# Kernel optimization log

Measured on AMD Instinct MI355X. Metric: run time of the kernel, lower is better.

Reference implementation:

```python
import jax, jax.numpy as jnp
import numpy as np

N, L, C, H = 8, 2048, 512, 512
C_HALF = max(C // 2, 1)


def setup_inputs() -> dict:
    key = jax.random.key(0)
    ks = jax.random.split(key, 11)
    s = 0.02
    return {
        "x": jax.random.normal(ks[0], (N, L, C), dtype=jnp.float32),
        "theta_w": jax.random.normal(ks[1], (C, H), dtype=jnp.float32) * s,
        "theta_b": jax.random.normal(ks[2], (H,), dtype=jnp.float32) * s,
        "phi_w": jax.random.normal(ks[3], (C, H), dtype=jnp.float32) * s,
        "phi_b": jax.random.normal(ks[4], (H,), dtype=jnp.float32) * s,
        "psi_w": jax.random.normal(ks[5], (C, H), dtype=jnp.float32) * s,
        "psi_b": jax.random.normal(ks[6], (H,), dtype=jnp.float32) * s,
        "r1_w": jax.random.normal(ks[7], (H, C_HALF), dtype=jnp.float32) * s,
        "r1_b": jax.random.normal(ks[8], (C_HALF,), dtype=jnp.float32) * s,
        "r2_w": jax.random.normal(ks[9], (C_HALF, C), dtype=jnp.float32) * s,
        "r2_b": jax.random.normal(ks[10], (C,), dtype=jnp.float32) * s,
    }


def reference(x, theta_w, theta_b, phi_w, phi_b, psi_w, psi_b, r1_w, r1_b, r2_w, r2_b):
    # projections: [n, L, h]
    x_t = x @ theta_w + theta_b
    x_ph = x @ phi_w + phi_b
    x_psi = x @ psi_w + psi_b
    # unscaled attention: phi @ theta^T -> [n, L, L], softmax over last dim
    attn = jax.nn.softmax(jnp.einsum("nlh,nmh->nlm", x_ph, x_t), axis=2)
    x_add = jnp.einsum("nlm,nmh->nlh", attn, x_psi)
    # recover MLP with LeakyReLU(0.2) then Tanh, residual add
    h1 = jax.nn.leaky_relu(x_add @ r1_w + r1_b, negative_slope=0.2)
    h2 = jnp.tanh(h1 @ r2_w + r2_b)
    return x + h2
```

## Files before the change

### kernel.cpp

```cpp
#include <hip/hip_runtime.h>
#include <hip/hip_bf16.h>

typedef __bf16 bf16x8 __attribute__((ext_vector_type(8)));
typedef float  f32x4  __attribute__((ext_vector_type(4)));
typedef __attribute__((address_space(3))) unsigned int       lds_uint;
typedef __attribute__((address_space(1))) const unsigned int glb_uint;

__device__ __forceinline__ unsigned short f2bf(float f) {
    unsigned int u = __float_as_uint(f);
    u += 0x7fffu + ((u >> 16) & 1u);
    return (unsigned short)(u >> 16);
}
__device__ __forceinline__ float tanh_fast(float x) {
    float e = __expf(-2.0f * fabsf(x));
    float r = (1.0f - e) / (1.0f + e);
    return copysignf(r, x);
}
__device__ __forceinline__ unsigned char f2fp8(float v) {
    return (unsigned char)(__builtin_amdgcn_cvt_pk_fp8_f32(v, 0.0f, 0, false) & 0xff);
}

__global__ __launch_bounds__(256) void prep(
    const float* __restrict__ x,
    const float* __restrict__ theta_w, const float* __restrict__ phi_w,
    const float* __restrict__ psi_w,   const float* __restrict__ r1_w,
    const float* __restrict__ r2_w,
    const float* __restrict__ theta_b, const float* __restrict__ phi_b,
    const float* __restrict__ psi_b,
    unsigned char* __restrict__ xb8, unsigned char* __restrict__ wCat8T,
    unsigned short* __restrict__ r1T, unsigned short* __restrict__ r2T,
    float* __restrict__ bCat) {
    const int b = blockIdx.x, t = threadIdx.x;
    if (b < 8192) {
        long i = ((long)b * 256 + t) * 4;
        float4 f = *(const float4*)(x + i);
        int w = __builtin_amdgcn_cvt_pk_fp8_f32(f.x, f.y, 0, false);
        w = __builtin_amdgcn_cvt_pk_fp8_f32(f.z, f.w, w, true);
        *(unsigned int*)(xb8 + i) = (unsigned int)w;
    } else if (b < 11264) {
        const int sel = (b - 8192) >> 10;
        const int idx = ((b - 8192) & 1023) * 256 + t;
        const float* w = sel == 0 ? theta_w : (sel == 1 ? phi_w : psi_w);
        const int r = idx >> 9, c = idx & 511;
        wCat8T[(long)(sel * 512 + c) * 512 + r] = f2fp8(w[idx] * 16.0f);
    } else if (b < 11776) {
        const int idx = (b - 11264) * 256 + t;
        const int r = idx >> 8, c = idx & 255;
        r1T[(long)c * 512 + r] = f2bf(r1_w[idx]);
    } else if (b < 12288) {
        const int idx = (b - 11776) * 256 + t;
        const int r = idx >> 9, c = idx & 511;
        r2T[(long)c * 256 + r] = f2bf(r2_w[idx]);
    } else {
        const int i = (b - 12288) * 256 + t;
        if (i < 1536)
            bCat[i] = i < 512 ? theta_b[i] : (i < 1024 ? phi_b[i - 512] : psi_b[i - 1024]);
    }
}

__global__ __launch_bounds__(256) void softmax_fp8(unsigned short* __restrict__ S) {
    const size_t row = (size_t)blockIdx.y * 2048 + blockIdx.x;
    unsigned short* p = S + row * 2048;
    const int t = threadIdx.x;
    uint4 raw = *(uint4*)(p + t * 8);
    unsigned int w[4] = {raw.x, raw.y, raw.z, raw.w};
    float v[8];
#pragma unroll
    for (int i = 0; i < 4; ++i) {
        v[2 * i]     = __uint_as_float((w[i] & 0xffffu) << 16);
        v[2 * i + 1] = __uint_as_float(w[i] & 0xffff0000u);
    }
    float mx = v[0];
#pragma unroll
    for (int i = 1; i < 8; ++i) mx = fmaxf(mx, v[i]);
#pragma unroll
    for (int off = 32; off > 0; off >>= 1) mx = fmaxf(mx, __shfl_xor(mx, off));
    __shared__ float red[8];
    const int wave = t >> 6, lane = t & 63;
    if (lane == 0) red[wave] = mx;
    __syncthreads();
    mx = fmaxf(fmaxf(red[0], red[1]), fmaxf(red[2], red[3]));
    float s = 0.0f;
#pragma unroll
    for (int i = 0; i < 8; ++i) { v[i] = __expf(v[i] - mx); s += v[i]; }
#pragma unroll
    for (int off = 32; off > 0; off >>= 1) s += __shfl_xor(s, off);
    if (lane == 0) red[4 + wave] = s;
    __syncthreads();
    s = red[4] + red[5] + red[6] + red[7];
    const float inv = 1.0f / s;
    int o0 = __builtin_amdgcn_cvt_pk_fp8_f32(v[0] * inv, v[1] * inv, 0, false);
    o0 = __builtin_amdgcn_cvt_pk_fp8_f32(v[2] * inv, v[3] * inv, o0, true);
    int o1 = __builtin_amdgcn_cvt_pk_fp8_f32(v[4] * inv, v[5] * inv, 0, false);
    o1 = __builtin_amdgcn_cvt_pk_fp8_f32(v[6] * inv, v[7] * inv, o1, true);
    uint2 ov; ov.x = (unsigned int)o0; ov.y = (unsigned int)o1;
    *(uint2*)((unsigned char*)p + t * 8) = ov;
}

template <int MODE>
__global__ __launch_bounds__(256) void gemm_fp8(
    const unsigned char* __restrict__ A,
    const unsigned char* __restrict__ Bt,
    const float* __restrict__ bias,
    unsigned short* __restrict__ outB,
    unsigned char* __restrict__ outT,
    unsigned char* __restrict__ outP,
    unsigned char* __restrict__ outV,
    int K, int ldaB, int ldbB, int ldc, long sA, long sB, long sC) {
    __shared__ unsigned char As[128 * 128];
    __shared__ unsigned char Bs[128 * 128];

    const int tid  = threadIdx.x;
    const int lane = tid & 63, wave = tid >> 6;
    const int m16  = lane & 15, quad = lane >> 4;
    const int wm   = (wave >> 1) << 6, wn = (wave & 1) << 6;
    const int m0   = blockIdx.x << 7, n0 = blockIdx.y << 7;

    const int srow = lane >> 3;
    const int uswz = (lane & 7) ^ srow;

    const unsigned char* Abase = A  + (long)blockIdx.z * sA + (long)m0 * ldaB;
    const unsigned char* Bbase = Bt + (long)blockIdx.z * sB + (long)n0 * ldbB;
    const int stR = (wave << 5) + srow;
    const long gA0 = (long)stR * ldaB + (uswz << 4);
    const long gB0 = (long)stR * ldbB + (uswz << 4);

    f32x4 acc[4][4] = {};

    for (int k0 = 0; k0 < K; k0 += 128) {
        __syncthreads();
#pragma unroll
        for (int i = 0; i < 4; ++i) {
            const unsigned char* gp = Abase + gA0 + (long)(i << 3) * ldaB + k0;
            unsigned char* lp = &As[(((wave << 5) + (i << 3)) << 7)];
            __builtin_amdgcn_global_load_lds((glb_uint*)gp, (lds_uint*)lp, 16, 0, 0);
        }
#pragma unroll
        for (int i = 0; i < 4; ++i) {
            const unsigned char* gp = Bbase + gB0 + (long)(i << 3) * ldbB + k0;
            unsigned char* lp = &Bs[(((wave << 5) + (i << 3)) << 7)];
            __builtin_amdgcn_global_load_lds((glb_uint*)gp, (lds_uint*)lp, 16, 0, 0);
        }
        __syncthreads();
#pragma unroll
        for (int ks = 0; ks < 4; ++ks) {
            long af[4], bg[4];
#pragma unroll
            for (int f = 0; f < 4; ++f) {
                const int m = wm + (f << 4) + m16;
                const int n = wn + (f << 4) + m16;
                const int c = (ks << 2) + quad;
                af[f] = *(const long*)&As[(m << 7) + ((c ^ ((m & 7) << 1)) << 3)];
                bg[f] = *(const long*)&Bs[(n << 7) + ((c ^ ((n & 7) << 1)) << 3)];
            }
#pragma unroll
            for (int fi = 0; fi < 4; ++fi)
#pragma unroll
                for (int fj = 0; fj < 4; ++fj)
                    acc[fi][fj] = __builtin_amdgcn_mfma_f32_16x16x32_fp8_fp8(
                        af[fi], bg[fj], acc[fi][fj], 0, 0, 0);
        }
    }

    const long zC = (long)blockIdx.z * sC;
#pragma unroll
    for (int fj = 0; fj < 4; ++fj) {
        const int col = n0 + wn + (fj << 4) + m16;
        float bv = 0.0f;
        if (MODE == 0) bv = bias[col];
#pragma unroll
        for (int fi = 0; fi < 4; ++fi) {
#pragma unroll
            for (int r = 0; r < 4; ++r) {
                const int row = m0 + wm + (fi << 4) + (quad << 2) + r;
                if (MODE == 0) {
                    const float v = acc[fi][fj][r] * 0.0625f + bv;
                    const unsigned char b8 = f2fp8(v);
                    const int sel = col >> 9, cb = col & 511;
                    if (sel == 0)      outT[(long)row * 512 + cb] = b8;
                    else if (sel == 1) outP[(long)row * 512 + cb] = b8;
                    else {
                        const int z = row >> 11, l = row & 2047;
                        outV[((long)z * 512 + cb) * 2048 + l] = b8;
                    }
                } else {
                    outB[zC + (long)row * ldc + col] = f2bf(acc[fi][fj][r]);
                }
            }
        }
    }
}

template <int MODE>
__global__ __launch_bounds__(256) void gemm128(
    const unsigned short* __restrict__ A,
    const unsigned short* __restrict__ Bt,
    const float* __restrict__ bias,
    const float* __restrict__ resid,
    unsigned short* __restrict__ outB,
    float* __restrict__ outF,
    int K, int lda, int ldb, int ldc) {
    __shared__ __bf16 As[128 * 64];
    __shared__ __bf16 Bs[128 * 64];

    const int tid  = threadIdx.x;
    const int lane = tid & 63, wave = tid >> 6;
    const int m16  = lane & 15, quad = lane >> 4;
    const int wm   = (wave >> 1) << 6, wn = (wave & 1) << 6;
    const int m0   = blockIdx.x << 7, n0 = blockIdx.y << 7;

    const int srow  = lane >> 3;
    const int uswz  = (lane & 7) ^ srow;

    const unsigned short* Abase = A  + (long)m0 * lda;
    const unsigned short* Bbase = Bt + (long)n0 * ldb;
    const int stR = (wave << 5) + srow;
    const long gA0 = (long)stR * lda + (uswz << 3);
    const long gB0 = (long)stR * ldb + (uswz << 3);

    f32x4 acc[4][4] = {};

    for (int k0 = 0; k0 < K; k0 += 64) {
        __syncthreads();
#pragma unroll
        for (int i = 0; i < 4; ++i) {
            const unsigned short* gp = Abase + gA0 + (long)(i << 3) * lda + k0;
            __bf16* lp = &As[(((wave << 5) + (i << 3)) << 6)];
            __builtin_amdgcn_global_load_lds((glb_uint*)gp, (lds_uint*)lp, 16, 0, 0);
        }
#pragma unroll
        for (int i = 0; i < 4; ++i) {
            const unsigned short* gp = Bbase + gB0 + (long)(i << 3) * ldb + k0;
            __bf16* lp = &Bs[(((wave << 5) + (i << 3)) << 6)];
            __builtin_amdgcn_global_load_lds((glb_uint*)gp, (lds_uint*)lp, 16, 0, 0);
        }
        __syncthreads();
#pragma unroll
        for (int ks = 0; ks < 2; ++ks) {
            bf16x8 af[4], bg[4];
#pragma unroll
            for (int f = 0; f < 4; ++f) {
                const int m  = wm + (f << 4) + m16;
                const int n  = wn + (f << 4) + m16;
                const int cu = (ks << 2) + quad;
                af[f] = *(const bf16x8*)&As[(m << 6) + ((cu ^ (m & 7)) << 3)];
                bg[f] = *(const bf16x8*)&Bs[(n << 6) + ((cu ^ (n & 7)) << 3)];
            }
#pragma unroll
            for (int fi = 0; fi < 4; ++fi)
#pragma unroll
                for (int fj = 0; fj < 4; ++fj)
                    acc[fi][fj] = __builtin_amdgcn_mfma_f32_16x16x32_bf16(
                        af[fi], bg[fj], acc[fi][fj], 0, 0, 0);
        }
    }

#pragma unroll
    for (int fj = 0; fj < 4; ++fj) {
        const int col = n0 + wn + (fj << 4) + m16;
        const float bv = bias[col];
#pragma unroll
        for (int fi = 0; fi < 4; ++fi) {
#pragma unroll
            for (int r = 0; r < 4; ++r) {
                const int row = m0 + wm + (fi << 4) + (quad << 2) + r;
                float v = acc[fi][fj][r] + bv;
                const long idx = (long)row * ldc + col;
                if (MODE == 2) {
                    v = v > 0.0f ? v : 0.2f * v;
                    outB[idx] = f2bf(v);
                } else {
                    outF[idx] = tanh_fast(v) + resid[idx];
                }
            }
        }
    }
}

extern "C" void kernel_launch(void* const* d_in, const int* in_sizes, int n_in,
                              void* d_out, int out_size, void* d_ws, size_t ws_size,
                              hipStream_t stream) {
    const float* x       = (const float*)d_in[0];
    const float* theta_w = (const float*)d_in[1];
    const float* theta_b = (const float*)d_in[2];
    const float* phi_w   = (const float*)d_in[3];
    const float* phi_b   = (const float*)d_in[4];
    const float* psi_w   = (const float*)d_in[5];
    const float* psi_b   = (const float*)d_in[6];
    const float* r1_w    = (const float*)d_in[7];
    const float* r1_b    = (const float*)d_in[8];
    const float* r2_w    = (const float*)d_in[9];
    const float* r2_b    = (const float*)d_in[10];
    float* out = (float*)d_out;

    constexpr int  N = 8, L = 2048, C = 512, H = 512, CH = 256;
    constexpr long NL = (long)N * L;

    char* p = (char*)d_ws;
    auto alloc = [&](size_t bytes) { void* q = (void*)p; p += bytes; return q; };
    unsigned char*  xb8    = (unsigned char*)alloc(NL * C);
    unsigned char*  TH8    = (unsigned char*)alloc(NL * H);
    unsigned char*  PH8    = (unsigned char*)alloc(NL * H);
    unsigned char*  VT8    = (unsigned char*)alloc((long)N * H * L);
    unsigned short* xadd   = (unsigned short*)alloc(NL * H * 2);
    unsigned short* h1     = (unsigned short*)alloc(NL * CH * 2);
    unsigned char*  wCat8T = (unsigned char*)alloc((long)1536 * 512);
    unsigned short* r1T    = (unsigned short*)alloc((long)H * CH * 2);
    unsigned short* r2T    = (unsigned short*)alloc((long)CH * C * 2);
    float*          bCat   = (float*)alloc(1536 * 4 + 256);
    unsigned short* S      = (unsigned short*)alloc((long)N * L * L * 2);

    prep<<<12294, 256, 0, stream>>>(x, theta_w, phi_w, psi_w, r1_w, r2_w,
                                    theta_b, phi_b, psi_b, xb8, wCat8T, r1T, r2T, bCat);

    gemm_fp8<0><<<dim3(NL / 128, 1536 / 128, 1), 256, 0, stream>>>(
        xb8, wCat8T, bCat, nullptr, TH8, PH8, VT8,
        C, C, C, 0, 0, 0, 0);

    gemm_fp8<1><<<dim3(L / 128, L / 128, N), 256, 0, stream>>>(
        PH8, TH8, nullptr, S, nullptr, nullptr, nullptr,
        H, H, H, L, (long)L * H, (long)L * H, (long)L * L);

    softmax_fp8<<<dim3(L, N), 256, 0, stream>>>(S);

    gemm_fp8<1><<<dim3(L / 128, H / 128, N), 256, 0, stream>>>(
        (const unsigned char*)S, VT8, nullptr, xadd, nullptr, nullptr, nullptr,
        L, 2 * L, L, H, (long)L * 2 * L, (long)H * L, (long)L * H);

    gemm128<2><<<dim3(NL / 128, CH / 128, 1), 256, 0, stream>>>(
        xadd, r1T, r1_b, nullptr, h1, nullptr, H, H, H, CH);

    gemm128<3><<<dim3(NL / 128, C / 128, 1), 256, 0, stream>>>(
        h1, r2T, r2_b, x, nullptr, out, CH, CH, CH, C);
}
```

Baseline: 262.5 us.

## Move recover MLP GEMMs to fp8, store scores as fp16, vectorize V-transpose stores

Quantizes the recover-MLP weights and intermediate activations (x_add, h1) to fp8, so the two MLP GEMMs run through the fp8 MFMA kernel instead of the bf16 one. The scores buffer changes from bf16 to fp16, and the projection epilogue for the V part now packs four fp8 values per 32-bit store instead of scattering single bytes. The aim is to halve the memory traffic and raise MFMA throughput in the tail GEMMs and to cut store transactions in the projection. In exchange it adds fp8 quantization error to the MLP path, and fp16 scores may overflow for large logits.

```diff
diff --git a/kernel.cpp b/kernel.cpp
--- a/kernel.cpp
+++ b/kernel.cpp
@@ -1,16 +1,10 @@
 #include <hip/hip_runtime.h>
 #include <hip/hip_bf16.h>
 
-typedef __bf16 bf16x8 __attribute__((ext_vector_type(8)));
-typedef float  f32x4  __attribute__((ext_vector_type(4)));
+typedef float f32x4 __attribute__((ext_vector_type(4)));
 typedef __attribute__((address_space(3))) unsigned int       lds_uint;
 typedef __attribute__((address_space(1))) const unsigned int glb_uint;
 
-__device__ __forceinline__ unsigned short f2bf(float f) {
-    unsigned int u = __float_as_uint(f);
-    u += 0x7fffu + ((u >> 16) & 1u);
-    return (unsigned short)(u >> 16);
-}
 __device__ __forceinline__ float tanh_fast(float x) {
     float e = __expf(-2.0f * fabsf(x));
     float r = (1.0f - e) / (1.0f + e);
@@ -18,6 +12,17 @@
 }
 __device__ __forceinline__ unsigned char f2fp8(float v) {
     return (unsigned char)(__builtin_amdgcn_cvt_pk_fp8_f32(v, 0.0f, 0, false) & 0xff);
+}
+__device__ __forceinline__ unsigned short f2h(float v) {
+    _Float16 h = (_Float16)v;
+    unsigned short u;
+    __builtin_memcpy(&u, &h, 2);
+    return u;
+}
+__device__ __forceinline__ float h2f(unsigned short u) {
+    _Float16 h;
+    __builtin_memcpy(&h, &u, 2);
+    return (float)h;
 }
 
 __global__ __launch_bounds__(256) void prep(
@@ -28,7 +33,7 @@
     const float* __restrict__ theta_b, const float* __restrict__ phi_b,
     const float* __restrict__ psi_b,
     unsigned char* __restrict__ xb8, unsigned char* __restrict__ wCat8T,
-    unsigned short* __restrict__ r1T, unsigned short* __restrict__ r2T,
+    unsigned char* __restrict__ r1T8, unsigned char* __restrict__ r2T8,
     float* __restrict__ bCat) {
     const int b = blockIdx.x, t = threadIdx.x;
     if (b < 8192) {
@@ -46,11 +51,11 @@
     } else if (b < 11776) {
         const int idx = (b - 11264) * 256 + t;
         const int r = idx >> 8, c = idx & 255;
-        r1T[(long)c * 512 + r] = f2bf(r1_w[idx]);
+        r1T8[(long)c * 512 + r] = f2fp8(r1_w[idx] * 16.0f);
     } else if (b < 12288) {
         const int idx = (b - 11776) * 256 + t;
         const int r = idx >> 9, c = idx & 511;
-        r2T[(long)c * 256 + r] = f2bf(r2_w[idx]);
+        r2T8[(long)c * 256 + r] = f2fp8(r2_w[idx] * 16.0f);
     } else {
         const int i = (b - 12288) * 256 + t;
         if (i < 1536)
@@ -67,8 +72,8 @@
     float v[8];
 #pragma unroll
     for (int i = 0; i < 4; ++i) {
-        v[2 * i]     = __uint_as_float((w[i] & 0xffffu) << 16);
-        v[2 * i + 1] = __uint_as_float(w[i] & 0xffff0000u);
+        v[2 * i]     = h2f((unsigned short)(w[i] & 0xffffu));
+        v[2 * i + 1] = h2f((unsigned short)(w[i] >> 16));
     }
     float mx = v[0];
 #pragma unroll
@@ -102,10 +107,12 @@
     const unsigned char* __restrict__ A,
     const unsigned char* __restrict__ Bt,
     const float* __restrict__ bias,
-    unsigned short* __restrict__ outB,
-    unsigned char* __restrict__ outT,
-    unsigned char* __restrict__ outP,
+    const float* __restrict__ resid,
+    unsigned short* __restrict__ outH,
+    unsigned char* __restrict__ out8,
+    unsigned char* __restrict__ out8b,
     unsigned char* __restrict__ outV,
+    float* __restrict__ outF,
     int K, int ldaB, int ldbB, int ldc, long sA, long sB, long sC) {
     __shared__ unsigned char As[128 * 128];
     __shared__ unsigned char Bs[128 * 128];
@@ -163,116 +170,68 @@
     }
 
     const long zC = (long)blockIdx.z * sC;
-#pragma unroll
-    for (int fj = 0; fj < 4; ++fj) {
-        const int col = n0 + wn + (fj << 4) + m16;
-        float bv = 0.0f;
-        if (MODE == 0) bv = bias[col];
-#pragma unroll
-        for (int fi = 0; fi < 4; ++fi) {
-#pragma unroll
-            for (int r = 0; r < 4; ++r) {
-                const int row = m0 + wm + (fi << 4) + (quad << 2) + r;
-                if (MODE == 0) {
-                    const float v = acc[fi][fj][r] * 0.0625f + bv;
-                    const unsigned char b8 = f2fp8(v);
-                    const int sel = col >> 9, cb = col & 511;
-                    if (sel == 0)      outT[(long)row * 512 + cb] = b8;
-                    else if (sel == 1) outP[(long)row * 512 + cb] = b8;
-                    else {
-                        const int z = row >> 11, l = row & 2047;
-                        outV[((long)z * 512 + cb) * 2048 + l] = b8;
+
+    if (MODE == 0) {
+        const int sel = n0 >> 9;
+        if (sel < 2) {
+            unsigned char* dst = sel == 0 ? out8 : out8b;
+#pragma unroll
+            for (int fj = 0; fj < 4; ++fj) {
+                const int col = n0 + wn + (fj << 4) + m16;
+                const int cb  = col & 511;
+                const float bv = bias[col];
+#pragma unroll
+                for (int fi = 0; fi < 4; ++fi)
+#pragma unroll
+                    for (int r = 0; r < 4; ++r) {
+                        const int row = m0 + wm + (fi << 4) + (quad << 2) + r;
+                        dst[(long)row * 512 + cb] = f2fp8(acc[fi][fj][r] * 0.0625f + bv);
                     }
-                } else {
-                    outB[zC + (long)row * ldc + col] = f2bf(acc[fi][fj][r]);
+            }
+        } else {
+            const int z = m0 >> 11, l0 = (m0 & 2047) + wm + (quad << 2);
+#pragma unroll
+            for (int fj = 0; fj < 4; ++fj) {
+                const int col = n0 + wn + (fj << 4) + m16;
+                const int h   = col & 511;
+                const float bv = bias[col];
+#pragma unroll
+                for (int fi = 0; fi < 4; ++fi) {
+                    int w = __builtin_amdgcn_cvt_pk_fp8_f32(
+                        acc[fi][fj][0] * 0.0625f + bv, acc[fi][fj][1] * 0.0625f + bv, 0, false);
+                    w = __builtin_amdgcn_cvt_pk_fp8_f32(
+                        acc[fi][fj][2] * 0.0625f + bv, acc[fi][fj][3] * 0.0625f + bv, w, true);
+                    *(unsigned int*)(outV + ((long)z * 512 + h) * 2048 + l0 + (fi << 4)) =
+                        (unsigned int)w;
                 }
             }
         }
-    }
-}
-
-template <int MODE>
-__global__ __launch_bounds__(256) void gemm128(
-    const unsigned short* __restrict__ A,
-    const unsigned short* __restrict__ Bt,
-    const float* __restrict__ bias,
-    const float* __restrict__ resid,
-    unsigned short* __restrict__ outB,
-    float* __restrict__ outF,
-    int K, int lda, int ldb, int ldc) {
-    __shared__ __bf16 As[128 * 64];
-    __shared__ __bf16 Bs[128 * 64];
-
-    const int tid  = threadIdx.x;
-    const int lane = tid & 63, wave = tid >> 6;
-    const int m16  = lane & 15, quad = lane >> 4;
-    const int wm   = (wave >> 1) << 6, wn = (wave & 1) << 6;
-    const int m0   = blockIdx.x << 7, n0 = blockIdx.y << 7;
-
-    const int srow  = lane >> 3;
-    const int uswz  = (lane & 7) ^ srow;
-
-    const unsigned short* Abase = A  + (long)m0 * lda;
-    const unsigned short* Bbase = Bt + (long)n0 * ldb;
-    const int stR = (wave << 5) + srow;
-    const long gA0 = (long)stR * lda + (uswz << 3);
-    const long gB0 = (long)stR * ldb + (uswz << 3);
-
-    f32x4 acc[4][4] = {};
-
-    for (int k0 = 0; k0 < K; k0 += 64) {
-        __syncthreads();
-#pragma unroll
-        for (int i = 0; i < 4; ++i) {
-            const unsigned short* gp = Abase + gA0 + (long)(i << 3) * lda + k0;
-            __bf16* lp = &As[(((wave << 5) + (i << 3)) << 6)];
-            __builtin_amdgcn_global_load_lds((glb_uint*)gp, (lds_uint*)lp, 16, 0, 0);
-        }
-#pragma unroll
-        for (int i = 0; i < 4; ++i) {
-            const unsigned short* gp = Bbase + gB0 + (long)(i << 3) * ldb + k0;
-            __bf16* lp = &Bs[(((wave << 5) + (i << 3)) << 6)];
-            __builtin_amdgcn_global_load_lds((glb_uint*)gp, (lds_uint*)lp, 16, 0, 0);
-        }
-        __syncthreads();
-#pragma unroll
-        for (int ks = 0; ks < 2; ++ks) {
-            bf16x8 af[4], bg[4];
-#pragma unroll
-            for (int f = 0; f < 4; ++f) {
-                const int m  = wm + (f << 4) + m16;
-                const int n  = wn + (f << 4) + m16;
-                const int cu = (ks << 2) + quad;
-                af[f] = *(const bf16x8*)&As[(m << 6) + ((cu ^ (m & 7)) << 3)];
-                bg[f] = *(const bf16x8*)&Bs[(n << 6) + ((cu ^ (n & 7)) << 3)];
-            }
+    } else {
+#pragma unroll
+        for (int fj = 0; fj < 4; ++fj) {
+            const int col = n0 + wn + (fj << 4) + m16;
+            float bv = 0.0f;
+            if (MODE >= 3) bv = bias[col];
 #pragma unroll
             for (int fi = 0; fi < 4; ++fi)
 #pragma unroll
-                for (int fj = 0; fj < 4; ++fj)
-                    acc[fi][fj] = __builtin_amdgcn_mfma_f32_16x16x32_bf16(
-                        af[fi], bg[fj], acc[fi][fj], 0, 0, 0);
-        }
-    }
-
-#pragma unroll
-    for (int fj = 0; fj < 4; ++fj) {
-        const int col = n0 + wn + (fj << 4) + m16;
-        const float bv = bias[col];
-#pragma unroll
-        for (int fi = 0; fi < 4; ++fi) {
-#pragma unroll
-            for (int r = 0; r < 4; ++r) {
-                const int row = m0 + wm + (fi << 4) + (quad << 2) + r;
-                float v = acc[fi][fj][r] + bv;
-                const long idx = (long)row * ldc + col;
-                if (MODE == 2) {
-                    v = v > 0.0f ? v : 0.2f * v;
-                    outB[idx] = f2bf(v);
-                } else {
-                    outF[idx] = tanh_fast(v) + resid[idx];
+                for (int r = 0; r < 4; ++r) {
+                    const int row = m0 + wm + (fi << 4) + (quad << 2) + r;
+                    float v = acc[fi][fj][r];
+                    if (MODE == 1) {
+                        outH[zC + (long)row * ldc + col] = f2h(v);
+                    } else if (MODE == 2) {
+                        out8[zC + (long)row * 512 + col] = f2fp8(v);
+                    } else if (MODE == 3) {
+                        v = v * 0.0625f + bv;
+                        v = v > 0.0f ? v : 0.2f * v;
+                        out8[(long)row * 256 + col] = f2fp8(v);
+                    } else {
+                        v = v * 0.0625f + bv;
+                        const long idx = (long)row * ldc + col;
+                        outF[idx] = tanh_fast(v) + resid[idx];
+                    }
                 }
-            }
         }
     }
 }
@@ -302,34 +261,36 @@
     unsigned char*  TH8    = (unsigned char*)alloc(NL * H);
     unsigned char*  PH8    = (unsigned char*)alloc(NL * H);
     unsigned char*  VT8    = (unsigned char*)alloc((long)N * H * L);
-    unsigned short* xadd   = (unsigned short*)alloc(NL * H * 2);
-    unsigned short* h1     = (unsigned short*)alloc(NL * CH * 2);
+    unsigned char*  xadd8  = (unsigned char*)alloc(NL * H);
+    unsigned char*  h18    = (unsigned char*)alloc(NL * CH);
     unsigned char*  wCat8T = (unsigned char*)alloc((long)1536 * 512);
-    unsigned short* r1T    = (unsigned short*)alloc((long)H * CH * 2);
-    unsigned short* r2T    = (unsigned short*)alloc((long)CH * C * 2);
+    unsigned char*  r1T8   = (unsigned char*)alloc((long)H * CH);
+    unsigned char*  r2T8   = (unsigned char*)alloc((long)CH * C);
     float*          bCat   = (float*)alloc(1536 * 4 + 256);
     unsigned short* S      = (unsigned short*)alloc((long)N * L * L * 2);
 
     prep<<<12294, 256, 0, stream>>>(x, theta_w, phi_w, psi_w, r1_w, r2_w,
-                                    theta_b, phi_b, psi_b, xb8, wCat8T, r1T, r2T, bCat);
+                                    theta_b, phi_b, psi_b, xb8, wCat8T, r1T8, r2T8, bCat);
 
     gemm_fp8<0><<<dim3(NL / 128, 1536 / 128, 1), 256, 0, stream>>>(
-        xb8, wCat8T, bCat, nullptr, TH8, PH8, VT8,
+        xb8, wCat8T, bCat, nullptr, nullptr, TH8, PH8, VT8, nullptr,
         C, C, C, 0, 0, 0, 0);
 
     gemm_fp8<1><<<dim3(L / 128, L / 128, N), 256, 0, stream>>>(
-        PH8, TH8, nullptr, S, nullptr, nullptr, nullptr,
+        PH8, TH8, nullptr, nullptr, S, nullptr, nullptr, nullptr, nullptr,
         H, H, H, L, (long)L * H, (long)L * H, (long)L * L);
 
     softmax_fp8<<<dim3(L, N), 256, 0, stream>>>(S);
 
-    gemm_fp8<1><<<dim3(L / 128, H / 128, N), 256, 0, stream>>>(
-        (const unsigned char*)S, VT8, nullptr, xadd, nullptr, nullptr, nullptr,
+    gemm_fp8<2><<<dim3(L / 128, H / 128, N), 256, 0, stream>>>(
+        (const unsigned char*)S, VT8, nullptr, nullptr, nullptr, xadd8, nullptr, nullptr, nullptr,
         L, 2 * L, L, H, (long)L * 2 * L, (long)H * L, (long)L * H);
 
-    gemm128<2><<<dim3(NL / 128, CH / 128, 1), 256, 0, stream>>>(
-        xadd, r1T, r1_b, nullptr, h1, nullptr, H, H, H, CH);
-
-    gemm128<3><<<dim3(NL / 128, C / 128, 1), 256, 0, stream>>>(
-        h1, r2T, r2_b, x, nullptr, out, CH, CH, CH, C);
-}
+    gemm_fp8<3><<<dim3(NL / 128, CH / 128, 1), 256, 0, stream>>>(
+        xadd8, r1T8, r1_b, nullptr, nullptr, h18, nullptr, nullptr, nullptr,
+        H, H, H, CH, 0, 0, 0);
+
+    gemm_fp8<4><<<dim3(NL / 128, C / 128, 1), 256, 0, stream>>>(
+        h18, r2T8, r2_b, x, nullptr, nullptr, nullptr, nullptr, out,
+        CH, CH, CH, C, 0, 0, 0);
+}
```

After: 245.1 us. 6.6% less time.
